# Kernel tuning notes

Hardware: AMD Instinct MI355X
Metric: run time of the kernel (lower is better)

The kernel has to match this reference:

```python
import jax, jax.numpy as jnp
import numpy as np

EPS = 1e-5  # eps placed on the diagonal via the 'eye' buffer in the torch module


def setup_inputs() -> dict:
    key = jax.random.key(0)
    k1, k2, k3 = jax.random.split(key, 3)
    B, C, H, W = 32, 256, 64, 64
    F = C // 4
    x = jax.random.normal(k1, (B, C, H, W), dtype=jnp.float32)
    # affine mixing weight [4,4,F] (torch inits diag(0.5,1,1,1); we add noise to exercise all paths)
    weight = jnp.eye(4, dtype=jnp.float32)[:, :, None] * jnp.ones((F,), jnp.float32) \
             + 0.1 * jax.random.normal(k2, (4, 4, F), dtype=jnp.float32)
    bias = 0.1 * jax.random.normal(k3, (4, F), dtype=jnp.float32)
    return {"x": x, "weight": weight, "bias": bias}


def reference(x, weight, bias):
    B, C, H, W = x.shape
    F = C // 4
    # split channels into 4 quaternion components: [4, B, F, H, W]
    xq = x.reshape(B, 4, F, H, W).transpose(1, 0, 2, 3, 4)
    # per (component, channel) mean over batch+spatial
    mean = xq.mean(axis=(1, 3, 4))                       # [4, F]
    xc = xq - mean[:, None, :, None, None]               # centered
    N = B * H * W
    # covariance across the 4 quaternion components, per channel: [F, 4, 4]
    v = xc.transpose(2, 0, 1, 3, 4).reshape(F, 4, N)     # [F, 4, N]
    cov = jnp.einsum('fin,fjn->fij', v, v) / N
    # batched 4x4 Cholesky and lower-triangular whitening solve
    L = jnp.linalg.cholesky(cov + EPS * jnp.eye(4, dtype=x.dtype))  # [F, 4, 4]
    z = jax.scipy.linalg.solve_triangular(L, v, lower=True)         # [F, 4, N]
    z = z.reshape(F, 4, B, H, W).transpose(1, 2, 0, 3, 4)           # [4, B, F, H, W]
    # unrolled 4x4 affine mix + bias, per channel
    out = jnp.einsum('ijf,jbfhw->ibfhw', weight, z) + bias[:, None, :, None, None]
    # re-concatenate components along channels -> [B, C, H, W]
    return out.transpose(1, 0, 2, 3, 4).reshape(B, C, H, W)
```

## Files before the change

kernel.cpp:

```cpp
#include <hip/hip_runtime.h>
#include <math.h>

constexpr int B   = 32;
constexpr int C   = 256;
constexpr int F   = 64;
constexpr int HW  = 64 * 64;
constexpr int HW4 = HW / 4;
constexpr int P4  = B * HW4;
constexpr float EPSV = 1e-5f;

constexpr int SBLOCKS = 32;
constexpr int SITER   = P4 / (SBLOCKS * 256);
constexpr int TBLOCKS = P4 / 256;

typedef float f32x4 __attribute__((ext_vector_type(4)));

__global__ __launch_bounds__(256) void stats_kernel(const float* __restrict__ x,
                                                    float* __restrict__ sums) {
    const int f     = blockIdx.x / SBLOCKS;
    const int chunk = blockIdx.x % SBLOCKS;
    const int tid   = threadIdx.x;

    float acc[14];
#pragma unroll
    for (int i = 0; i < 14; ++i) acc[i] = 0.f;

    const float4* xb = reinterpret_cast<const float4*>(x);

#pragma unroll
    for (int it = 0; it < SITER; ++it) {
        const int p   = chunk * (256 * SITER) + it * 256 + tid;
        const int b   = p >> 10;
        const int hw4 = p & (HW4 - 1);
        float4 v[4];
#pragma unroll
        for (int q = 0; q < 4; ++q)
            v[q] = xb[(size_t)(b * C + q * F + f) * HW4 + hw4];
#pragma unroll
        for (int l = 0; l < 4; ++l) {
            float e0 = ((const float*)&v[0])[l];
            float e1 = ((const float*)&v[1])[l];
            float e2 = ((const float*)&v[2])[l];
            float e3 = ((const float*)&v[3])[l];
            acc[0] += e0; acc[1] += e1; acc[2] += e2; acc[3] += e3;
            acc[4]  += e0 * e0; acc[5]  += e0 * e1; acc[6]  += e0 * e2; acc[7]  += e0 * e3;
            acc[8]  += e1 * e1; acc[9]  += e1 * e2; acc[10] += e1 * e3;
            acc[11] += e2 * e2; acc[12] += e2 * e3;
            acc[13] += e3 * e3;
        }
    }

#pragma unroll
    for (int i = 0; i < 14; ++i) {
#pragma unroll
        for (int off = 32; off >= 1; off >>= 1)
            acc[i] += __shfl_down(acc[i], off, 64);
    }

    __shared__ float red[4][14];
    const int wave = tid >> 6;
    const int lane = tid & 63;
    if (lane == 0) {
#pragma unroll
        for (int i = 0; i < 14; ++i) red[wave][i] = acc[i];
    }
    __syncthreads();
    if (tid < 14) {
        float t = red[0][tid] + red[1][tid] + red[2][tid] + red[3][tid];
        atomicAdd(&sums[f * 14 + tid], t);
    }
}

__global__ __launch_bounds__(256) void transform_kernel(
    const float* __restrict__ x,
    const float* __restrict__ sums,
    const float* __restrict__ weight,
    const float* __restrict__ bias,
    float* __restrict__ out)
{
    const int f     = blockIdx.x >> 7;
    const int chunk = blockIdx.x & (TBLOCKS - 1);

    const int p   = chunk * 256 + threadIdx.x;
    const int b   = p >> 10;
    const int hw4 = p & (HW4 - 1);

    const float4* xb = reinterpret_cast<const float4*>(x);
    f32x4*        ob = reinterpret_cast<f32x4*>(out);

    float4 v[4];
#pragma unroll
    for (int q = 0; q < 4; ++q)
        v[q] = xb[(size_t)(b * C + q * F + f) * HW4 + hw4];

    const float invN = 1.0f / (float)(B * HW);

    float s14[14];
#pragma unroll
    for (int i = 0; i < 14; ++i) s14[i] = sums[f * 14 + i];

    float m[4];
#pragma unroll
    for (int q = 0; q < 4; ++q) m[q] = s14[q] * invN;

    float cov[4][4];
    {
        int k = 4;
#pragma unroll
        for (int i = 0; i < 4; ++i)
#pragma unroll
            for (int j = i; j < 4; ++j) {
                float cij = s14[k] * invN - m[i] * m[j];
                cov[i][j] = cij;
                cov[j][i] = cij;
                ++k;
            }
    }
#pragma unroll
    for (int i = 0; i < 4; ++i) cov[i][i] += EPSV;

    float L[4][4] = {};
#pragma unroll
    for (int i = 0; i < 4; ++i) {
#pragma unroll
        for (int j = 0; j <= i; ++j) {
            float s = cov[i][j];
#pragma unroll
            for (int k = 0; k < j; ++k) s -= L[i][k] * L[j][k];
            if (i == j) L[i][j] = sqrtf(s);
            else        L[i][j] = s / L[j][j];
        }
    }
    float Li[4][4] = {};
#pragma unroll
    for (int j = 0; j < 4; ++j) {
        Li[j][j] = 1.0f / L[j][j];
#pragma unroll
        for (int i = j + 1; i < 4; ++i) {
            float s = 0.f;
#pragma unroll
            for (int k = j; k < i; ++k) s += L[i][k] * Li[k][j];
            Li[i][j] = -s / L[i][i];
        }
    }
    float M[4][4];
#pragma unroll
    for (int i = 0; i < 4; ++i)
#pragma unroll
        for (int j = 0; j < 4; ++j) {
            float s = 0.f;
#pragma unroll
            for (int k = 0; k < 4; ++k)
                s += weight[(i * 4 + k) * F + f] * Li[k][j];
            M[i][j] = s;
        }
    float cvec[4];
#pragma unroll
    for (int i = 0; i < 4; ++i) {
        float ci = bias[i * F + f];
#pragma unroll
        for (int j = 0; j < 4; ++j) ci -= M[i][j] * m[j];
        cvec[i] = ci;
    }

#pragma unroll
    for (int i = 0; i < 4; ++i) {
        const float m0 = M[i][0], m1 = M[i][1], m2 = M[i][2], m3 = M[i][3];
        const float ci = cvec[i];
        f32x4 o;
        o.x = ci + m0 * v[0].x + m1 * v[1].x + m2 * v[2].x + m3 * v[3].x;
        o.y = ci + m0 * v[0].y + m1 * v[1].y + m2 * v[2].y + m3 * v[3].y;
        o.z = ci + m0 * v[0].z + m1 * v[1].z + m2 * v[2].z + m3 * v[3].z;
        o.w = ci + m0 * v[0].w + m1 * v[1].w + m2 * v[2].w + m3 * v[3].w;
        __builtin_nontemporal_store(o, &ob[(size_t)(b * C + i * F + f) * HW4 + hw4]);
    }
}

extern "C" void kernel_launch(void* const* d_in, const int* in_sizes, int n_in,
                              void* d_out, int out_size, void* d_ws, size_t ws_size,
                              hipStream_t stream) {
    const float* x      = (const float*)d_in[0];
    const float* weight = (const float*)d_in[1];
    const float* bias   = (const float*)d_in[2];
    float*       out    = (float*)d_out;

    float* sums = (float*)d_ws;

    hipMemsetAsync(sums, 0, F * 14 * sizeof(float), stream);
    stats_kernel<<<F * SBLOCKS, 256, 0, stream>>>(x, sums);
    transform_kernel<<<F * TBLOCKS, 256, 0, stream>>>(x, sums, weight, bias, out);
}
```

Baseline: 254.7 us.

## Replace atomic stats with per-block partials and process one batch image per transform block

The stats kernel now writes per-block partial sums to workspace instead of atomically adding, which removes the memset launch and the atomics. The transform kernel reduces the 32 partials itself and solves the 4x4 whitening once per block. Each block now covers a whole batch image (4 chunks per thread, with software-pipelined loads), so the number of transform blocks drops 4x and the per-block solve is amortized. The old atomic path is kept as a fallback when the workspace is too small.

New measurement: 253.0 us. About the same (-0.7%).

```diff
diff --git a/kernel.cpp b/kernel.cpp
--- a/kernel.cpp
+++ b/kernel.cpp
@@ -11,12 +11,13 @@
 
 constexpr int SBLOCKS = 32;
 constexpr int SITER   = P4 / (SBLOCKS * 256);
-constexpr int TBLOCKS = P4 / 256;
+constexpr int TBLK    = 32;
+constexpr int TITER   = P4 / (TBLK * 256);
 
 typedef float f32x4 __attribute__((ext_vector_type(4)));
 
 __global__ __launch_bounds__(256) void stats_kernel(const float* __restrict__ x,
-                                                    float* __restrict__ sums) {
+                                                    float* __restrict__ partial) {
     const int f     = blockIdx.x / SBLOCKS;
     const int chunk = blockIdx.x % SBLOCKS;
     const int tid   = threadIdx.x;
@@ -67,11 +68,204 @@
     __syncthreads();
     if (tid < 14) {
         float t = red[0][tid] + red[1][tid] + red[2][tid] + red[3][tid];
+        partial[(size_t)(f * SBLOCKS + chunk) * 14 + tid] = t;
+    }
+}
+
+__device__ __forceinline__ void solve_from_sums(
+    const float* __restrict__ s14, int f,
+    const float* __restrict__ weight, const float* __restrict__ bias,
+    float M[4][4], float cvec[4])
+{
+    const float invN = 1.0f / (float)(B * HW);
+
+    float m[4];
+#pragma unroll
+    for (int q = 0; q < 4; ++q) m[q] = s14[q] * invN;
+
+    float cov[4][4];
+    {
+        int k = 4;
+#pragma unroll
+        for (int i = 0; i < 4; ++i)
+#pragma unroll
+            for (int j = i; j < 4; ++j) {
+                float cij = s14[k] * invN - m[i] * m[j];
+                cov[i][j] = cij;
+                cov[j][i] = cij;
+                ++k;
+            }
+    }
+#pragma unroll
+    for (int i = 0; i < 4; ++i) cov[i][i] += EPSV;
+
+    float L[4][4] = {};
+#pragma unroll
+    for (int i = 0; i < 4; ++i) {
+#pragma unroll
+        for (int j = 0; j <= i; ++j) {
+            float s = cov[i][j];
+#pragma unroll
+            for (int k = 0; k < j; ++k) s -= L[i][k] * L[j][k];
+            if (i == j) L[i][j] = sqrtf(s);
+            else        L[i][j] = s / L[j][j];
+        }
+    }
+    float Li[4][4] = {};
+#pragma unroll
+    for (int j = 0; j < 4; ++j) {
+        Li[j][j] = 1.0f / L[j][j];
+#pragma unroll
+        for (int i = j + 1; i < 4; ++i) {
+            float s = 0.f;
+#pragma unroll
+            for (int k = j; k < i; ++k) s += L[i][k] * Li[k][j];
+            Li[i][j] = -s / L[i][i];
+        }
+    }
+#pragma unroll
+    for (int i = 0; i < 4; ++i)
+#pragma unroll
+        for (int j = 0; j < 4; ++j) {
+            float s = 0.f;
+#pragma unroll
+            for (int k = 0; k < 4; ++k)
+                s += weight[(i * 4 + k) * F + f] * Li[k][j];
+            M[i][j] = s;
+        }
+#pragma unroll
+    for (int i = 0; i < 4; ++i) {
+        float ci = bias[i * F + f];
+#pragma unroll
+        for (int j = 0; j < 4; ++j) ci -= M[i][j] * m[j];
+        cvec[i] = ci;
+    }
+}
+
+__global__ __launch_bounds__(256) void transform_kernel(
+    const float* __restrict__ x,
+    const float* __restrict__ partial,
+    const float* __restrict__ weight,
+    const float* __restrict__ bias,
+    float* __restrict__ out)
+{
+    const int f     = blockIdx.x >> 5;
+    const int chunk = blockIdx.x & (TBLK - 1);
+    const int tid   = threadIdx.x;
+    const int b     = chunk;
+
+    const float4* xb = reinterpret_cast<const float4*>(x);
+    f32x4*        ob = reinterpret_cast<f32x4*>(out);
+
+    size_t plane[4];
+#pragma unroll
+    for (int q = 0; q < 4; ++q)
+        plane[q] = (size_t)(b * C + q * F + f) * HW4;
+
+    float4 va[4], vb[4];
+#pragma unroll
+    for (int q = 0; q < 4; ++q) va[q] = xb[plane[q] + tid];
+
+    __shared__ float s14[14];
+    if (tid < 14) {
+        const float* pp = partial + (size_t)f * SBLOCKS * 14 + tid;
+        float s = 0.f;
+#pragma unroll
+        for (int c = 0; c < SBLOCKS; ++c) s += pp[c * 14];
+        s14[tid] = s;
+    }
+    __syncthreads();
+
+    float M[4][4], cvec[4];
+    float s14r[14];
+#pragma unroll
+    for (int i = 0; i < 14; ++i) s14r[i] = s14[i];
+    solve_from_sums(s14r, f, weight, bias, M, cvec);
+
+#define APPLY(V, IT)                                                          \
+    {                                                                         \
+        const int hw4 = (IT) * 256 + tid;                                     \
+        _Pragma("unroll")                                                     \
+        for (int i = 0; i < 4; ++i) {                                         \
+            const float m0 = M[i][0], m1 = M[i][1], m2 = M[i][2], m3 = M[i][3]; \
+            const float ci = cvec[i];                                         \
+            f32x4 o;                                                          \
+            o.x = ci + m0 * V[0].x + m1 * V[1].x + m2 * V[2].x + m3 * V[3].x; \
+            o.y = ci + m0 * V[0].y + m1 * V[1].y + m2 * V[2].y + m3 * V[3].y; \
+            o.z = ci + m0 * V[0].z + m1 * V[1].z + m2 * V[2].z + m3 * V[3].z; \
+            o.w = ci + m0 * V[0].w + m1 * V[1].w + m2 * V[2].w + m3 * V[3].w; \
+            __builtin_nontemporal_store(o, &ob[plane[i] + hw4]);              \
+        }                                                                     \
+    }
+
+#pragma unroll
+    for (int q = 0; q < 4; ++q) vb[q] = xb[plane[q] + 256 + tid];
+    APPLY(va, 0);
+#pragma unroll
+    for (int q = 0; q < 4; ++q) va[q] = xb[plane[q] + 512 + tid];
+    APPLY(vb, 1);
+#pragma unroll
+    for (int q = 0; q < 4; ++q) vb[q] = xb[plane[q] + 768 + tid];
+    APPLY(va, 2);
+    APPLY(vb, 3);
+#undef APPLY
+}
+
+__global__ __launch_bounds__(256) void stats_atomic_kernel(const float* __restrict__ x,
+                                                           float* __restrict__ sums) {
+    const int f     = blockIdx.x / SBLOCKS;
+    const int chunk = blockIdx.x % SBLOCKS;
+    const int tid   = threadIdx.x;
+
+    float acc[14];
+#pragma unroll
+    for (int i = 0; i < 14; ++i) acc[i] = 0.f;
+
+    const float4* xb = reinterpret_cast<const float4*>(x);
+
+#pragma unroll
+    for (int it = 0; it < SITER; ++it) {
+        const int p   = chunk * (256 * SITER) + it * 256 + tid;
+        const int b   = p >> 10;
+        const int hw4 = p & (HW4 - 1);
+        float4 v[4];
+#pragma unroll
+        for (int q = 0; q < 4; ++q)
+            v[q] = xb[(size_t)(b * C + q * F + f) * HW4 + hw4];
+#pragma unroll
+        for (int l = 0; l < 4; ++l) {
+            float e0 = ((const float*)&v[0])[l];
+            float e1 = ((const float*)&v[1])[l];
+            float e2 = ((const float*)&v[2])[l];
+            float e3 = ((const float*)&v[3])[l];
+            acc[0] += e0; acc[1] += e1; acc[2] += e2; acc[3] += e3;
+            acc[4]  += e0 * e0; acc[5]  += e0 * e1; acc[6]  += e0 * e2; acc[7]  += e0 * e3;
+            acc[8]  += e1 * e1; acc[9]  += e1 * e2; acc[10] += e1 * e3;
+            acc[11] += e2 * e2; acc[12] += e2 * e3;
+            acc[13] += e3 * e3;
+        }
+    }
+#pragma unroll
+    for (int i = 0; i < 14; ++i) {
+#pragma unroll
+        for (int off = 32; off >= 1; off >>= 1)
+            acc[i] += __shfl_down(acc[i], off, 64);
+    }
+    __shared__ float red[4][14];
+    const int wave = tid >> 6;
+    const int lane = tid & 63;
+    if (lane == 0) {
+#pragma unroll
+        for (int i = 0; i < 14; ++i) red[wave][i] = acc[i];
+    }
+    __syncthreads();
+    if (tid < 14) {
+        float t = red[0][tid] + red[1][tid] + red[2][tid] + red[3][tid];
         atomicAdd(&sums[f * 14 + tid], t);
     }
 }
 
-__global__ __launch_bounds__(256) void transform_kernel(
+__global__ __launch_bounds__(256) void transform1_kernel(
     const float* __restrict__ x,
     const float* __restrict__ sums,
     const float* __restrict__ weight,
@@ -79,11 +273,10 @@
     float* __restrict__ out)
 {
     const int f     = blockIdx.x >> 7;
-    const int chunk = blockIdx.x & (TBLOCKS - 1);
-
-    const int p   = chunk * 256 + threadIdx.x;
-    const int b   = p >> 10;
-    const int hw4 = p & (HW4 - 1);
+    const int chunk = blockIdx.x & 127;
+    const int p     = chunk * 256 + threadIdx.x;
+    const int b     = p >> 10;
+    const int hw4   = p & (HW4 - 1);
 
     const float4* xb = reinterpret_cast<const float4*>(x);
     f32x4*        ob = reinterpret_cast<f32x4*>(out);
@@ -93,75 +286,12 @@
     for (int q = 0; q < 4; ++q)
         v[q] = xb[(size_t)(b * C + q * F + f) * HW4 + hw4];
 
-    const float invN = 1.0f / (float)(B * HW);
-
     float s14[14];
 #pragma unroll
     for (int i = 0; i < 14; ++i) s14[i] = sums[f * 14 + i];
 
-    float m[4];
-#pragma unroll
-    for (int q = 0; q < 4; ++q) m[q] = s14[q] * invN;
-
-    float cov[4][4];
-    {
-        int k = 4;
-#pragma unroll
-        for (int i = 0; i < 4; ++i)
-#pragma unroll
-            for (int j = i; j < 4; ++j) {
-                float cij = s14[k] * invN - m[i] * m[j];
-                cov[i][j] = cij;
-                cov[j][i] = cij;
-                ++k;
-            }
-    }
-#pragma unroll
-    for (int i = 0; i < 4; ++i) cov[i][i] += EPSV;
-
-    float L[4][4] = {};
-#pragma unroll
-    for (int i = 0; i < 4; ++i) {
-#pragma unroll
-        for (int j = 0; j <= i; ++j) {
-            float s = cov[i][j];
-#pragma unroll
-            for (int k = 0; k < j; ++k) s -= L[i][k] * L[j][k];
-            if (i == j) L[i][j] = sqrtf(s);
-            else        L[i][j] = s / L[j][j];
-        }
-    }
-    float Li[4][4] = {};
-#pragma unroll
-    for (int j = 0; j < 4; ++j) {
-        Li[j][j] = 1.0f / L[j][j];
-#pragma unroll
-        for (int i = j + 1; i < 4; ++i) {
-            float s = 0.f;
-#pragma unroll
-            for (int k = j; k < i; ++k) s += L[i][k] * Li[k][j];
-            Li[i][j] = -s / L[i][i];
-        }
-    }
-    float M[4][4];
-#pragma unroll
-    for (int i = 0; i < 4; ++i)
-#pragma unroll
-        for (int j = 0; j < 4; ++j) {
-            float s = 0.f;
-#pragma unroll
-            for (int k = 0; k < 4; ++k)
-                s += weight[(i * 4 + k) * F + f] * Li[k][j];
-            M[i][j] = s;
-        }
-    float cvec[4];
-#pragma unroll
-    for (int i = 0; i < 4; ++i) {
-        float ci = bias[i * F + f];
-#pragma unroll
-        for (int j = 0; j < 4; ++j) ci -= M[i][j] * m[j];
-        cvec[i] = ci;
-    }
+    float M[4][4], cvec[4];
+    solve_from_sums(s14, f, weight, bias, M, cvec);
 
 #pragma unroll
     for (int i = 0; i < 4; ++i) {
@@ -184,9 +314,15 @@
     const float* bias   = (const float*)d_in[2];
     float*       out    = (float*)d_out;
 
-    float* sums = (float*)d_ws;
-
-    hipMemsetAsync(sums, 0, F * 14 * sizeof(float), stream);
-    stats_kernel<<<F * SBLOCKS, 256, 0, stream>>>(x, sums);
-    transform_kernel<<<F * TBLOCKS, 256, 0, stream>>>(x, sums, weight, bias, out);
-}
+    const size_t need = (size_t)F * SBLOCKS * 14 * sizeof(float);
+    if (ws_size >= need) {
+        float* partial = (float*)d_ws;
+        stats_kernel<<<F * SBLOCKS, 256, 0, stream>>>(x, partial);
+        transform_kernel<<<F * TBLK, 256, 0, stream>>>(x, partial, weight, bias, out);
+    } else {
+        float* sums = (float*)d_ws;
+        hipMemsetAsync(sums, 0, F * 14 * sizeof(float), stream);
+        stats_atomic_kernel<<<F * SBLOCKS, 256, 0, stream>>>(x, sums);
+        transform1_kernel<<<F * 128, 256, 0, stream>>>(x, sums, weight, bias, out);
+    }
+}
```
